# Kernel optimization log

Measured on AMD Instinct MI355X. Metric: run time of the kernel, lower is better.

## Reference

```python
import jax, jax.numpy as jnp
import numpy as np

B, LV, LS = 16, 512, 512
FEA_V, FEA_S = 2048, 768
D_MODEL, H, DK, DV = 1024, 16, 64, 64
EPS = 1e-6


def setup_inputs() -> dict:
    key = jax.random.key(0)
    ks = jax.random.split(key, 16)
    sc = lambda fan_in: 1.0 / np.sqrt(fan_in)
    return {
        "v": jax.random.normal(ks[0], (B, LV, FEA_V), jnp.float32),
        "s": jax.random.normal(ks[1], (B, LS, FEA_S), jnp.float32),
        "W_lv": jax.random.normal(ks[2], (FEA_V, D_MODEL), jnp.float32) * sc(FEA_V),
        "b_lv": jnp.zeros((D_MODEL,), jnp.float32),
        "W_ls": jax.random.normal(ks[3], (FEA_S, D_MODEL), jnp.float32) * sc(FEA_S),
        "b_ls": jnp.zeros((D_MODEL,), jnp.float32),
        "pos_v": jax.random.normal(ks[4], (1, LV, D_MODEL), jnp.float32),
        "pos_s": jax.random.normal(ks[5], (1, LS, D_MODEL), jnp.float32),
        "W_q": jax.random.normal(ks[6], (D_MODEL, H * DK), jnp.float32) * sc(D_MODEL),
        "b_q": jnp.zeros((H * DK,), jnp.float32),
        "W_k": jax.random.normal(ks[7], (D_MODEL, H * DK), jnp.float32) * sc(D_MODEL),
        "b_k": jnp.zeros((H * DK,), jnp.float32),
        "W_v": jax.random.normal(ks[8], (D_MODEL, H * DV), jnp.float32) * sc(D_MODEL),
        "b_v": jnp.zeros((H * DV,), jnp.float32),
        "W_p": jax.random.normal(ks[9], (H * DV, D_MODEL), jnp.float32) * sc(H * DV),
        "b_p": jnp.zeros((D_MODEL,), jnp.float32),
        "ln_gamma": jnp.ones((D_MODEL,), jnp.float32),
        "ln_beta": jnp.zeros((D_MODEL,), jnp.float32),
        "v_len": LV,
        "s_len": LS,
    }


def _layer_norm(x, gamma, beta):
    mu = jnp.mean(x, axis=-1, keepdims=True)
    var = jnp.var(x, axis=-1, keepdims=True)
    return gamma * (x - mu) / jnp.sqrt(var + EPS) + beta


def reference(v, s, W_lv, b_lv, W_ls, b_ls, pos_v, pos_s, W_q, b_q, W_k, b_k,
              W_v, b_v, W_p, b_p, ln_gamma, ln_beta, v_len, s_len):
    b_size = v.shape[0]
    # input projections + ReLU (dropout is identity at eval)
    v = jax.nn.relu(v @ W_lv + b_lv)  # [B, LV, D]
    s = jax.nn.relu(s @ W_ls + b_ls)  # [B, LS, D]
    # positional embedding add (pos=True)
    residual_v = v + pos_v[:, : v.shape[1], :]
    # QKV projections; note the original unpack `q_v, k_s, k_s = ...`
    # overwrites the key with the VALUE projection of s, so both key and
    # value in attention are v_s (the W_v projection of s). W_k output is
    # computed in torch but discarded.
    q = (v @ W_q + b_q).reshape(b_size, -1, H, DK).transpose(0, 2, 1, 3)   # [B,H,LV,DK]
    _k = (s @ W_k + b_k)  # computed then discarded, kept for faithfulness
    vs = (s @ W_v + b_v).reshape(b_size, -1, H, DV).transpose(0, 2, 1, 3)  # [B,H,LS,DV]
    scores = jnp.einsum("bhqd,bhkd->bhqk", q, vs) / jnp.sqrt(jnp.float32(DK))
    attn = jax.nn.softmax(scores, axis=-1)
    context = jnp.einsum("bhqk,bhkd->bhqd", attn, vs)  # [B,H,LV,DV]
    context = context.transpose(0, 2, 1, 3).reshape(b_size, -1, H * DV)
    output_v = context @ W_p + b_p  # dropout identity at eval
    return _layer_norm(residual_v + output_v, ln_gamma, ln_beta)
```

## Files before the change

### kernel.cpp

```cpp
#include <hip/hip_runtime.h>

typedef unsigned short u16;
typedef unsigned int   u32;

using bf16x8 = __attribute__((ext_vector_type(8))) short;
using f32x4  = __attribute__((ext_vector_type(4))) float;

#define MFMA16(a, b, c) __builtin_amdgcn_mfma_f32_16x16x32_bf16((a), (b), (c), 0, 0, 0)

__device__ __forceinline__ u16 f2bf(float f) {
  union { float f; u32 u; } x; x.f = f;
  u32 r = x.u + 0x7fffu + ((x.u >> 16) & 1u);
  return (u16)(r >> 16);
}

__device__ __forceinline__ float bf2f(u16 v) {
  union { u32 u; float f; } x; x.u = ((u32)v) << 16;
  return x.f;
}

__device__ __forceinline__ u32 cvtpk(float lo, float hi) {
  u32 r;
  asm("v_cvt_pk_bf16_f32 %0, %1, %2" : "=v"(r) : "v"(lo), "v"(hi));
  return r;
}

__device__ __forceinline__ void gl2lds16(const void* g, void* l) {
  __builtin_amdgcn_global_load_lds(
      (const __attribute__((address_space(1))) u32*)g,
      (__attribute__((address_space(3))) u32*)l, 16, 0, 0);
}

__global__ __launch_bounds__(256) void cvt_f32_bf16(const float* __restrict__ in,
                                                    u16* __restrict__ out, long n8) {
  long i = (long)blockIdx.x * 256 + threadIdx.x;
  if (i >= n8) return;
  const float4* p = (const float4*)(in + i * 8);
  float4 a = p[0], b = p[1];
  uint4 pk;
  pk.x = cvtpk(a.x, a.y);
  pk.y = cvtpk(a.z, a.w);
  pk.z = cvtpk(b.x, b.y);
  pk.w = cvtpk(b.z, b.w);
  *(uint4*)(out + i * 8) = pk;
}

__global__ __launch_bounds__(256) void wt_cvt_t(const float* __restrict__ W,
                                                u16* __restrict__ Wt, int K, int N) {
  __shared__ u16 t[64][66];
  int tilesN = N >> 6;
  int k0 = ((int)blockIdx.x / tilesN) << 6;
  int n0 = ((int)blockIdx.x % tilesN) << 6;
  int tid = threadIdx.x;
  int c4 = (tid & 15) * 4, r16 = tid >> 4;
#pragma unroll
  for (int p = 0; p < 4; ++p) {
    int row = r16 + p * 16;
    float4 f = *(const float4*)(W + (size_t)(k0 + row) * N + n0 + c4);
    t[row][c4 + 0] = f2bf(f.x);
    t[row][c4 + 1] = f2bf(f.y);
    t[row][c4 + 2] = f2bf(f.z);
    t[row][c4 + 3] = f2bf(f.w);
  }
  __syncthreads();
  int c8 = (tid & 7) * 8, r32 = tid >> 3;
#pragma unroll
  for (int p = 0; p < 2; ++p) {
    int n = r32 + p * 32;
    u16 tmp[8] __attribute__((aligned(16)));
#pragma unroll
    for (int e = 0; e < 8; ++e) tmp[e] = t[c8 + e][n];
    *(uint4*)(Wt + (size_t)(n0 + n) * K + k0 + c8) = *(uint4*)tmp;
  }
}

template <int MODE>
__global__ __launch_bounds__(256) void gemm_bf16(
    const u16* __restrict__ A, const u16* __restrict__ Bt,
    const float* __restrict__ bias, u16* __restrict__ outb, float* __restrict__ outf,
    u16* __restrict__ outt, const u16* __restrict__ add0b,
    const float* __restrict__ add1, int M, int N, int K) {
  __shared__ u16 sA[128 * 64];
  __shared__ u16 sB[128 * 64];
  int tilesN = N >> 7;
  int nwg = (int)gridDim.x;
  int cpx = nwg >> 3;
  int orig = (int)blockIdx.x;
  int wg = (orig & 7) * cpx + (orig >> 3);
  int tm = wg / tilesN, tn = wg % tilesN;
  int m0 = tm << 7, n0 = tn << 7;
  int tid = threadIdx.x, w = tid >> 6, l = tid & 63;
  int wm = (w >> 1) << 6, wn = (w & 1) << 6;
  int c16 = l & 15, g16 = (l >> 4) * 16;

  f32x4 acc[4][4];
#pragma unroll
  for (int i = 0; i < 4; ++i)
#pragma unroll
    for (int j = 0; j < 4; ++j) acc[i][j] = (f32x4){0.f, 0.f, 0.f, 0.f};

  int nk = K >> 6;
  for (int kt = 0; kt < nk; ++kt) {
    __syncthreads();
    const u16* Ab = A + (size_t)m0 * K + kt * 64;
    const u16* Bb = Bt + (size_t)n0 * K + kt * 64;
#pragma unroll
    for (int j = 0; j < 4; ++j) {
      int chunk = w * 4 + j;
      int lin = chunk * 1024 + l * 16;
      int row = lin >> 7;
      int cb = (lin & 127) ^ ((row & 7) << 4);
      gl2lds16(Ab + (size_t)row * K + (cb >> 1), (char*)sA + chunk * 1024);
      gl2lds16(Bb + (size_t)row * K + (cb >> 1), (char*)sB + chunk * 1024);
    }
    __syncthreads();
#pragma unroll
    for (int kk = 0; kk < 2; ++kk) {
      bf16x8 af[4], bfr[4];
#pragma unroll
      for (int i = 0; i < 4; ++i) {
        int ar = wm + i * 16 + c16;
        af[i] = *(const bf16x8*)((const char*)sA + ar * 128 +
                                 ((kk * 64 + g16) ^ ((ar & 7) << 4)));
        int br = wn + i * 16 + c16;
        bfr[i] = *(const bf16x8*)((const char*)sB + br * 128 +
                                  ((kk * 64 + g16) ^ ((br & 7) << 4)));
      }
#pragma unroll
      for (int i = 0; i < 4; ++i)
#pragma unroll
        for (int j = 0; j < 4; ++j) acc[i][j] = MFMA16(af[i], bfr[j], acc[i][j]);
    }
  }
#pragma unroll
  for (int i = 0; i < 4; ++i) {
#pragma unroll
    for (int j = 0; j < 4; ++j) {
      float vv[4];
      int gn = n0 + wn + j * 16 + c16;
#pragma unroll
      for (int r = 0; r < 4; ++r) vv[r] = acc[i][j][r] + bias[gn];
      int gm0 = m0 + wm + i * 16 + (l >> 4) * 4;
      if (MODE == 0) {
#pragma unroll
        for (int r = 0; r < 4; ++r)
          outb[(size_t)(gm0 + r) * N + gn] = f2bf(fmaxf(vv[r], 0.f));
      } else if (MODE == 2 || MODE == 4) {
        int hh = gn >> 6, dk = gn & 63, bb2 = gm0 >> 9, ll2 = gm0 & 511;
#pragma unroll
        for (int r = 0; r < 4; ++r)
          outb[(((size_t)bb2 * 16 + hh) * 512 + ll2 + r) * 64 + dk] = f2bf(vv[r]);
        if (MODE == 4) {
          uint2 tw;
          tw.x = cvtpk(vv[0], vv[1]);
          tw.y = cvtpk(vv[2], vv[3]);
          *(uint2*)(outt + (((size_t)bb2 * 16 + hh) * 64 + dk) * 512 + ll2) = tw;
        }
      } else {
#pragma unroll
        for (int r = 0; r < 4; ++r) {
          int gm = gm0 + r;
          float v = vv[r] + bf2f(add0b[(size_t)gm * N + gn]) +
                    add1[(size_t)(gm & 511) * N + gn];
          outf[(size_t)gm * N + gn] = v;
        }
      }
    }
  }
}

__global__ __launch_bounds__(512) void attn_kernel(const u16* __restrict__ q,
                                                   const u16* __restrict__ kv,
                                                   const u16* __restrict__ kvT,
                                                   u16* __restrict__ ctx) {
  __shared__ u16 sK[2][4096];
  __shared__ u16 sVT[2][4096];
  __shared__ u16 sP[8192];

  int orig = (int)blockIdx.x;
  int r = (orig & 7) * 128 + (orig >> 3);
  int bh = r >> 2, qt = r & 3;
  int b = bh >> 4, h = bh & 15;
  int tid = threadIdx.x, w = tid >> 6, l = tid & 63;
  int c16 = l & 15, hi = l >> 4, g16 = hi * 16;
  int swzq = (c16 & 7) << 4;

  const u16* qbase = q + (size_t)bh * 32768 + (size_t)qt * 8192;
#pragma unroll
  for (int j = 0; j < 2; ++j) {
    int chunk = w * 2 + j;
    int lin = chunk * 1024 + l * 16;
    int row = lin >> 7;
    int cb = (lin & 127) ^ ((row & 7) << 4);
    gl2lds16(qbase + (size_t)row * 64 + (cb >> 1), (char*)sP + chunk * 1024);
  }
  {
    const u16* kb = kv + (size_t)bh * 32768;
    const u16* vb = kvT + (size_t)bh * 32768;
    int lin = w * 1024 + l * 16;
    int row = lin >> 7;
    int cb = (lin & 127) ^ ((row & 7) << 4);
    gl2lds16(kb + (size_t)row * 64 + (cb >> 1), (char*)sK[0] + w * 1024);
    gl2lds16(vb + (size_t)row * 512 + (cb >> 1), (char*)sVT[0] + w * 1024);
  }
  __syncthreads();

  const char* sQrow = (const char*)sP + (w * 16 + c16) * 128;
  bf16x8 qf0 = *(const bf16x8*)(sQrow + ((0 + g16) ^ swzq));
  bf16x8 qf1 = *(const bf16x8*)(sQrow + ((64 + g16) ^ swzq));

  char* sPw = (char*)sP + w * 2048;
  f32x4 of[4];
#pragma unroll
  for (int n = 0; n < 4; ++n) of[n] = (f32x4){0.f, 0.f, 0.f, 0.f};
  float m_run = -1e30f, l_run = 0.f;

  for (int c = 0; c < 8; ++c) {
    int cur = c & 1;
    if (c < 7) {
      const u16* kb = kv + (size_t)bh * 32768 + (size_t)(c + 1) * 4096;
      const u16* vb = kvT + (size_t)bh * 32768 + (c + 1) * 64;
      int lin = w * 1024 + l * 16;
      int row = lin >> 7;
      int cb = (lin & 127) ^ ((row & 7) << 4);
      gl2lds16(kb + (size_t)row * 64 + (cb >> 1), (char*)sK[cur ^ 1] + w * 1024);
      gl2lds16(vb + (size_t)row * 512 + (cb >> 1), (char*)sVT[cur ^ 1] + w * 1024);
    }
    const char* kbuf = (const char*)sK[cur];
    const char* vtbuf = (const char*)sVT[cur];

    f32x4 sf[4];
#pragma unroll
    for (int n = 0; n < 4; ++n) {
      const char* krow = kbuf + (n * 16 + c16) * 128;
      bf16x8 k0 = *(const bf16x8*)(krow + (g16 ^ swzq));
      bf16x8 k1 = *(const bf16x8*)(krow + ((64 + g16) ^ swzq));
      f32x4 z = (f32x4){0.f, 0.f, 0.f, 0.f};
      z = MFMA16(k0, qf0, z);
      z = MFMA16(k1, qf1, z);
      sf[n] = z;
    }

    float pmax = -1e30f;
#pragma unroll
    for (int n = 0; n < 4; ++n)
#pragma unroll
      for (int rr = 0; rr < 4; ++rr) {
        sf[n][rr] *= 0.125f;
        pmax = fmaxf(pmax, sf[n][rr]);
      }
    pmax = fmaxf(pmax, __shfl_xor(pmax, 16));
    pmax = fmaxf(pmax, __shfl_xor(pmax, 32));
    float mnew = fmaxf(m_run, pmax);
    float corr = __expf(m_run - mnew);
    float psum = 0.f;
#pragma unroll
    for (int n = 0; n < 4; ++n)
#pragma unroll
      for (int rr = 0; rr < 4; ++rr) {
        float p = __expf(sf[n][rr] - mnew);
        sf[n][rr] = p;
        psum += p;
      }
    psum += __shfl_xor(psum, 16);
    psum += __shfl_xor(psum, 32);
    l_run = l_run * corr + psum;
    m_run = mnew;
#pragma unroll
    for (int n = 0; n < 4; ++n)
#pragma unroll
      for (int rr = 0; rr < 4; ++rr) of[n][rr] *= corr;

#pragma unroll
    for (int n = 0; n < 4; ++n) {
      uint2 pw;
      pw.x = cvtpk(sf[n][0], sf[n][1]);
      pw.y = cvtpk(sf[n][2], sf[n][3]);
      *(uint2*)(sPw + c16 * 128 + ((n * 32 + hi * 8) ^ swzq)) = pw;
    }

    bf16x8 pf0 = *(const bf16x8*)(sPw + c16 * 128 + (g16 ^ swzq));
    bf16x8 pf1 = *(const bf16x8*)(sPw + c16 * 128 + ((64 + g16) ^ swzq));
#pragma unroll
    for (int n = 0; n < 4; ++n) {
      const char* vrow = vtbuf + (n * 16 + c16) * 128;
      bf16x8 v0 = *(const bf16x8*)(vrow + (g16 ^ swzq));
      bf16x8 v1 = *(const bf16x8*)(vrow + ((64 + g16) ^ swzq));
      of[n] = MFMA16(v0, pf0, of[n]);
      of[n] = MFMA16(v1, pf1, of[n]);
    }
    __syncthreads();
  }

  float inv = 1.0f / l_run;
  int grow = qt * 128 + w * 16 + c16;
  u16* obase = ctx + (size_t)(b * 512 + grow) * 1024 + h * 64;
#pragma unroll
  for (int n = 0; n < 4; ++n) {
    uint2 ow;
    ow.x = cvtpk(of[n][0] * inv, of[n][1] * inv);
    ow.y = cvtpk(of[n][2] * inv, of[n][3] * inv);
    *(uint2*)(obase + n * 16 + hi * 4) = ow;
  }
}

__global__ __launch_bounds__(256) void ln_kernel(float* __restrict__ x,
                                                 const float* __restrict__ gamma,
                                                 const float* __restrict__ beta) {
  __shared__ float red[4];
  __shared__ float red2[4];
  int row = blockIdx.x, tid = threadIdx.x;
  float4 v = *(float4*)(x + (size_t)row * 1024 + tid * 4);
  float s = v.x + v.y + v.z + v.w;
#pragma unroll
  for (int d = 1; d < 64; d <<= 1) s += __shfl_xor(s, d);
  if ((tid & 63) == 0) red[tid >> 6] = s;
  __syncthreads();
  float mu = (red[0] + red[1] + red[2] + red[3]) * (1.0f / 1024.0f);
  float d0 = v.x - mu, d1 = v.y - mu, d2 = v.z - mu, d3 = v.w - mu;
  float qq = d0 * d0 + d1 * d1 + d2 * d2 + d3 * d3;
#pragma unroll
  for (int d = 1; d < 64; d <<= 1) qq += __shfl_xor(qq, d);
  if ((tid & 63) == 0) red2[tid >> 6] = qq;
  __syncthreads();
  float var = (red2[0] + red2[1] + red2[2] + red2[3]) * (1.0f / 1024.0f);
  float rstd = rsqrtf(var + 1e-6f);
  float4 g = *(const float4*)(gamma + tid * 4);
  float4 bb = *(const float4*)(beta + tid * 4);
  v.x = g.x * d0 * rstd + bb.x;
  v.y = g.y * d1 * rstd + bb.y;
  v.z = g.z * d2 * rstd + bb.z;
  v.w = g.w * d3 * rstd + bb.w;
  *(float4*)(x + (size_t)row * 1024 + tid * 4) = v;
}

extern "C" void kernel_launch(void* const* d_in, const int* in_sizes, int n_in,
                              void* d_out, int out_size, void* d_ws, size_t ws_size,
                              hipStream_t stream) {
  (void)in_sizes; (void)n_in; (void)out_size; (void)ws_size;
  const float* v_in  = (const float*)d_in[0];
  const float* s_in  = (const float*)d_in[1];
  const float* W_lv  = (const float*)d_in[2];
  const float* b_lv  = (const float*)d_in[3];
  const float* W_ls  = (const float*)d_in[4];
  const float* b_ls  = (const float*)d_in[5];
  const float* pos_v = (const float*)d_in[6];
  const float* W_q   = (const float*)d_in[8];
  const float* b_q   = (const float*)d_in[9];
  const float* W_v   = (const float*)d_in[12];
  const float* b_v   = (const float*)d_in[13];
  const float* W_p   = (const float*)d_in[14];
  const float* b_p   = (const float*)d_in[15];
  const float* gamma = (const float*)d_in[16];
  const float* beta  = (const float*)d_in[17];
  float* out = (float*)d_out;

  char* ws = (char*)d_ws;
  size_t off = 0;
  auto alloc = [&](size_t bytes) {
    char* p = ws + off;
    off += (bytes + 255) & ~(size_t)255;
    return p;
  };
  u16* v_bf     = (u16*)alloc(33554432);
  u16* s_bf     = (u16*)alloc(12582912);
  u16* Wlv_t    = (u16*)alloc(4194304);
  u16* Wls_t    = (u16*)alloc(1572864);
  u16* Wq_t     = (u16*)alloc(2097152);
  u16* Wv_t     = (u16*)alloc(2097152);
  u16* Wp_t     = (u16*)alloc(2097152);
  u16* vproj_bf = (u16*)alloc(16777216);
  u16* sproj_bf = (u16*)alloc(16777216);
  u16* q_bf     = (u16*)alloc(16777216);
  u16* vs_bf    = (u16*)alloc(16777216);
  u16* vsT_bf   = (u16*)alloc(16777216);
  u16* ctx_bf   = (u16*)alloc(16777216);

  cvt_f32_bf16<<<8192, 256, 0, stream>>>(v_in, v_bf, 2097152);
  cvt_f32_bf16<<<3072, 256, 0, stream>>>(s_in, s_bf, 786432);
  wt_cvt_t<<<512, 256, 0, stream>>>(W_lv, Wlv_t, 2048, 1024);
  wt_cvt_t<<<192, 256, 0, stream>>>(W_ls, Wls_t, 768, 1024);
  wt_cvt_t<<<256, 256, 0, stream>>>(W_q, Wq_t, 1024, 1024);
  wt_cvt_t<<<256, 256, 0, stream>>>(W_v, Wv_t, 1024, 1024);
  wt_cvt_t<<<256, 256, 0, stream>>>(W_p, Wp_t, 1024, 1024);

  gemm_bf16<0><<<512, 256, 0, stream>>>(v_bf, Wlv_t, b_lv, vproj_bf, nullptr,
                                        nullptr, nullptr, nullptr, 8192, 1024, 2048);
  gemm_bf16<0><<<512, 256, 0, stream>>>(s_bf, Wls_t, b_ls, sproj_bf, nullptr,
                                        nullptr, nullptr, nullptr, 8192, 1024, 768);
  gemm_bf16<2><<<512, 256, 0, stream>>>(vproj_bf, Wq_t, b_q, q_bf, nullptr,
                                        nullptr, nullptr, nullptr, 8192, 1024, 1024);
  gemm_bf16<4><<<512, 256, 0, stream>>>(sproj_bf, Wv_t, b_v, vs_bf, nullptr,
                                        vsT_bf, nullptr, nullptr, 8192, 1024, 1024);
  attn_kernel<<<1024, 512, 0, stream>>>(q_bf, vs_bf, vsT_bf, ctx_bf);
  gemm_bf16<3><<<512, 256, 0, stream>>>(ctx_bf, Wp_t, b_p, nullptr, out,
                                        nullptr, vproj_bf, pos_v, 8192, 1024, 1024);
  ln_kernel<<<8192, 256, 0, stream>>>(out, gamma, beta);
}
```

Baseline: 235.9 us.

## Double-buffer GEMM LDS tiles and use 8 waves per workgroup

The bf16 GEMM now keeps two LDS buffers, so the global-to-LDS load of the next K tile overlaps the MFMA work on the current tile. This cuts the sync count per K step from two to one. The workgroup grows from 4 to 8 waves, each owning a 64x32 sub-tile instead of 64x64, which raises the number of waves available to hide latency. In exchange LDS use doubles to 64KB per block, which can cap how many blocks fit on a CU, and each wave gets less fragment reuse from LDS.

```diff
diff --git a/kernel.cpp b/kernel.cpp
--- a/kernel.cpp
+++ b/kernel.cpp
@@ -75,13 +75,13 @@
 }
 
 template <int MODE>
-__global__ __launch_bounds__(256) void gemm_bf16(
+__global__ __launch_bounds__(512) void gemm_bf16(
     const u16* __restrict__ A, const u16* __restrict__ Bt,
     const float* __restrict__ bias, u16* __restrict__ outb, float* __restrict__ outf,
     u16* __restrict__ outt, const u16* __restrict__ add0b,
     const float* __restrict__ add1, int M, int N, int K) {
-  __shared__ u16 sA[128 * 64];
-  __shared__ u16 sB[128 * 64];
+  __shared__ u16 sA[2][128 * 64];
+  __shared__ u16 sB[2][128 * 64];
   int tilesN = N >> 7;
   int nwg = (int)gridDim.x;
   int cpx = nwg >> 3;
@@ -90,57 +90,73 @@
   int tm = wg / tilesN, tn = wg % tilesN;
   int m0 = tm << 7, n0 = tn << 7;
   int tid = threadIdx.x, w = tid >> 6, l = tid & 63;
-  int wm = (w >> 1) << 6, wn = (w & 1) << 6;
-  int c16 = l & 15, g16 = (l >> 4) * 16;
-
-  f32x4 acc[4][4];
+  int wm = (w >> 2) << 6, wn = (w & 3) << 5;
+  int c16 = l & 15, hi = l >> 4, g16 = hi * 16;
+
+  f32x4 acc[4][2];
 #pragma unroll
   for (int i = 0; i < 4; ++i)
 #pragma unroll
-    for (int j = 0; j < 4; ++j) acc[i][j] = (f32x4){0.f, 0.f, 0.f, 0.f};
-
-  int nk = K >> 6;
-  for (int kt = 0; kt < nk; ++kt) {
-    __syncthreads();
+    for (int j = 0; j < 2; ++j) acc[i][j] = (f32x4){0.f, 0.f, 0.f, 0.f};
+
+  auto STAGE = [&](int kt, int buf) {
     const u16* Ab = A + (size_t)m0 * K + kt * 64;
     const u16* Bb = Bt + (size_t)n0 * K + kt * 64;
 #pragma unroll
-    for (int j = 0; j < 4; ++j) {
-      int chunk = w * 4 + j;
-      int lin = chunk * 1024 + l * 16;
+    for (int p = 0; p < 2; ++p) {
+      int lin = p * 8192 + tid * 16;
       int row = lin >> 7;
       int cb = (lin & 127) ^ ((row & 7) << 4);
-      gl2lds16(Ab + (size_t)row * K + (cb >> 1), (char*)sA + chunk * 1024);
-      gl2lds16(Bb + (size_t)row * K + (cb >> 1), (char*)sB + chunk * 1024);
-    }
-    __syncthreads();
+      int base = lin & ~1023;
+      gl2lds16(Ab + (size_t)row * K + (cb >> 1), (char*)sA[buf] + base);
+      gl2lds16(Bb + (size_t)row * K + (cb >> 1), (char*)sB[buf] + base);
+    }
+  };
+
+  auto COMPUTE = [&](int buf) {
 #pragma unroll
     for (int kk = 0; kk < 2; ++kk) {
-      bf16x8 af[4], bfr[4];
+      bf16x8 af[4], bfr[2];
 #pragma unroll
       for (int i = 0; i < 4; ++i) {
         int ar = wm + i * 16 + c16;
-        af[i] = *(const bf16x8*)((const char*)sA + ar * 128 +
+        af[i] = *(const bf16x8*)((const char*)sA[buf] + ar * 128 +
                                  ((kk * 64 + g16) ^ ((ar & 7) << 4)));
-        int br = wn + i * 16 + c16;
-        bfr[i] = *(const bf16x8*)((const char*)sB + br * 128 +
+      }
+#pragma unroll
+      for (int j = 0; j < 2; ++j) {
+        int br = wn + j * 16 + c16;
+        bfr[j] = *(const bf16x8*)((const char*)sB[buf] + br * 128 +
                                   ((kk * 64 + g16) ^ ((br & 7) << 4)));
       }
 #pragma unroll
       for (int i = 0; i < 4; ++i)
 #pragma unroll
-        for (int j = 0; j < 4; ++j) acc[i][j] = MFMA16(af[i], bfr[j], acc[i][j]);
-    }
-  }
+        for (int j = 0; j < 2; ++j) acc[i][j] = MFMA16(af[i], bfr[j], acc[i][j]);
+    }
+  };
+
+  int nk = K >> 6;
+  STAGE(0, 0);
+  __syncthreads();
+  int cur = 0;
+  for (int kt = 0; kt < nk - 1; ++kt) {
+    STAGE(kt + 1, cur ^ 1);
+    COMPUTE(cur);
+    __syncthreads();
+    cur ^= 1;
+  }
+  COMPUTE(cur);
+
 #pragma unroll
   for (int i = 0; i < 4; ++i) {
 #pragma unroll
-    for (int j = 0; j < 4; ++j) {
+    for (int j = 0; j < 2; ++j) {
       float vv[4];
       int gn = n0 + wn + j * 16 + c16;
 #pragma unroll
       for (int r = 0; r < 4; ++r) vv[r] = acc[i][j][r] + bias[gn];
-      int gm0 = m0 + wm + i * 16 + (l >> 4) * 4;
+      int gm0 = m0 + wm + i * 16 + hi * 4;
       if (MODE == 0) {
 #pragma unroll
         for (int r = 0; r < 4; ++r)
@@ -384,16 +400,16 @@
   wt_cvt_t<<<256, 256, 0, stream>>>(W_v, Wv_t, 1024, 1024);
   wt_cvt_t<<<256, 256, 0, stream>>>(W_p, Wp_t, 1024, 1024);
 
-  gemm_bf16<0><<<512, 256, 0, stream>>>(v_bf, Wlv_t, b_lv, vproj_bf, nullptr,
+  gemm_bf16<0><<<512, 512, 0, stream>>>(v_bf, Wlv_t, b_lv, vproj_bf, nullptr,
                                         nullptr, nullptr, nullptr, 8192, 1024, 2048);
-  gemm_bf16<0><<<512, 256, 0, stream>>>(s_bf, Wls_t, b_ls, sproj_bf, nullptr,
+  gemm_bf16<0><<<512, 512, 0, stream>>>(s_bf, Wls_t, b_ls, sproj_bf, nullptr,
                                         nullptr, nullptr, nullptr, 8192, 1024, 768);
-  gemm_bf16<2><<<512, 256, 0, stream>>>(vproj_bf, Wq_t, b_q, q_bf, nullptr,
+  gemm_bf16<2><<<512, 512, 0, stream>>>(vproj_bf, Wq_t, b_q, q_bf, nullptr,
                                         nullptr, nullptr, nullptr, 8192, 1024, 1024);
-  gemm_bf16<4><<<512, 256, 0, stream>>>(sproj_bf, Wv_t, b_v, vs_bf, nullptr,
+  gemm_bf16<4><<<512, 512, 0, stream>>>(sproj_bf, Wv_t, b_v, vs_bf, nullptr,
                                         vsT_bf, nullptr, nullptr, 8192, 1024, 1024);
   attn_kernel<<<1024, 512, 0, stream>>>(q_bf, vs_bf, vsT_bf, ctx_bf);
-  gemm_bf16<3><<<512, 256, 0, stream>>>(ctx_bf, Wp_t, b_p, nullptr, out,
+  gemm_bf16<3><<<512, 512, 0, stream>>>(ctx_bf, Wp_t, b_p, nullptr, out,
                                         nullptr, vproj_bf, pos_v, 8192, 1024, 1024);
   ln_kernel<<<8192, 256, 0, stream>>>(out, gamma, beta);
 }
```

Result: no change. 240.2 us (+1.8%).
